# Optimization experiments

Measured on AMD Instinct MI355X. Metric: run time of the kernel, lower is better.

The kernel has to match this reference:

```python
import jax, jax.numpy as jnp
import numpy as np

B, S, H = 64, 512, 768      # batch, subtokens, BERT hidden
N, E = 128, 1024            # word-nodes per graph, directed edges per graph
GH, FH, L = 128, 256, 2     # gnn_hidden, fc_hidden, num_labels


def setup_inputs() -> dict:
    key = jax.random.key(0)
    ks = jax.random.split(key, 14)
    p = lambda k, shp: 0.02 * jax.random.normal(k, shp, jnp.float32)
    return {
        "last_hidden": jax.random.normal(ks[0], (B, S, H), jnp.float32),
        "submap": jax.random.randint(ks[1], (B, S), 0, N, dtype=jnp.int32),
        "edge_index": jax.random.randint(ks[2], (B, 2, E), 0, N, dtype=jnp.int32),
        "num_nodes": N,
        "wr": p(ks[3], (H,)), "br": jnp.zeros((), jnp.float32),
        "W1": p(ks[4], (H, GH)), "b1": jnp.zeros((GH,), jnp.float32),
        "W2": p(ks[5], (GH, GH)), "b2": jnp.zeros((GH,), jnp.float32),
        "Wf1": p(ks[6], (H + GH, FH)), "bf1": jnp.zeros((FH,), jnp.float32),
        "Wf2": p(ks[7], (FH, L)), "bf2": jnp.zeros((L,), jnp.float32),
    }


def reference(last_hidden, submap, edge_index, num_nodes,
              wr, br, W1, b1, W2, b2, Wf1, bf1, Wf2, bf2):
    Bn, Sn, Hn = last_hidden.shape
    Nn = num_nodes
    BN = Bn * Nn

    # --- per-token rationale gating ---
    gate = jax.nn.sigmoid(jnp.einsum("bsh,h->bs", last_hidden, wr) + br)  # [B,S]
    gated = last_hidden * gate[..., None]                                  # [B,S,H]

    # --- subtoken -> word-node mean pooling (batched segment mean) ---
    offs = (jnp.arange(Bn, dtype=submap.dtype) * Nn)[:, None]
    seg = (submap + offs).reshape(-1)                     # [B*S] global node ids
    flat = gated.reshape(Bn * Sn, Hn)
    sums = jax.ops.segment_sum(flat, seg, num_segments=BN)
    cnts = jax.ops.segment_sum(jnp.ones((Bn * Sn,), flat.dtype), seg, num_segments=BN)
    node_feats = sums / jnp.maximum(cnts, 1.0)[:, None]   # zeros where no subtoken maps

    # --- batched GCN message passing (self-loops + PyG gcn_norm) ---
    eoffs = (jnp.arange(Bn, dtype=edge_index.dtype) * Nn)[:, None]
    src = (edge_index[:, 0, :] + eoffs).reshape(-1)       # [B*E]
    dst = (edge_index[:, 1, :] + eoffs).reshape(-1)
    self_idx = jnp.arange(BN, dtype=src.dtype)
    src_all = jnp.concatenate([src, self_idx])
    dst_all = jnp.concatenate([dst, self_idx])
    deg = jax.ops.segment_sum(jnp.ones_like(src_all, jnp.float32), dst_all, num_segments=BN)
    dinv = jax.lax.rsqrt(deg)                             # deg >= 1 due to self-loops
    norm = dinv[src_all] * dinv[dst_all]                  # [B*E + B*N]

    def gcn_layer(x, W, b):
        h = x @ W                                         # transform first (PyG GCNConv)
        msg = h[src_all] * norm[:, None]
        out = jax.ops.segment_sum(msg, dst_all, num_segments=BN) + b
        return jax.nn.relu(out)                           # relu applied in forward()

    x = gcn_layer(node_feats, W1, b1)
    x = gcn_layer(x, W2, b2)

    # --- graph mean pool, concat with CLS, classifier head (dropout = eval identity) ---
    pooled = x.reshape(Bn, Nn, -1).mean(axis=1)           # [B,GH]
    cls_emb = last_hidden[:, 0, :]                        # [B,H]
    h = jax.nn.relu(jnp.concatenate([cls_emb, pooled], axis=1) @ Wf1 + bf1)
    return h @ Wf2 + bf2                                  # [B,num_labels]
```

## Files before the change

### kernel.cpp

```cpp
#include <hip/hip_runtime.h>
#include <math.h>

#define Bz 64
#define Sz 512
#define Hz 768
#define Nz 128
#define Ez 1024
#define GHz 128
#define FHz 256
#define Lz 2
#define BNz (Bz * Nz)

typedef short bf16x8 __attribute__((ext_vector_type(8)));
typedef float f32x4  __attribute__((ext_vector_type(4)));
typedef unsigned short ushort;

__device__ inline ushort f2b(float f) {
    union { float f; unsigned u; } v; v.f = f;
    return (ushort)((v.u + 0x7FFFu + ((v.u >> 16) & 1u)) >> 16);
}

__global__ __launch_bounds__(256) void k_stage(
        const float* __restrict__ lh, const int* __restrict__ submap,
        const float* __restrict__ wr, const float* __restrict__ br,
        const float* __restrict__ W1, const float* __restrict__ W2,
        const int* __restrict__ ei,
        ushort* __restrict__ nfb, ushort* __restrict__ W1T, ushort* __restrict__ W2T,
        int* __restrict__ rowptrG, int* __restrict__ srcsG,
        float* __restrict__ wnG, float* __restrict__ dinvG) {
    int blk = blockIdx.x, t = threadIdx.x;
    __shared__ __align__(16) char arena[12288];

    if (blk >= 8192 && blk < 8576) {
        int i = (blk - 8192) * 256 + t;
        { int k = i >> 7, n = i & 127; W1T[n * Hz + k] = f2b(W1[i]); }
        if (i < GHz * GHz) { int k = i >> 7, n = i & 127; W2T[n * GHz + k] = f2b(W2[i]); }
        return;
    }
    if (blk >= 8576) {
        int b = blk - 8576;
        int*   srcl2 = (int*)arena;
        int*   dstl2 = (int*)(arena + 4096);
        int*   hist  = (int*)(arena + 8192);
        int*   off   = (int*)(arena + 8704);
        int*   rp    = (int*)(arena + 9216);
        float* di    = (float*)(arena + 9732);
        if (t < Nz) { hist[t] = 0; off[t] = 0; }
        __syncthreads();
        #pragma unroll
        for (int j = 0; j < 4; ++j) {
            int e = t + 256 * j;
            int s = ei[b * 2 * Ez + e], d = ei[b * 2 * Ez + Ez + e];
            srcl2[e] = s; dstl2[e] = d;
            atomicAdd(&hist[d], 1);
        }
        __syncthreads();
        if (t < Nz) {
            di[t] = rsqrtf((float)hist[t] + 1.0f);
            dinvG[b * Nz + t] = di[t];
        }
        __syncthreads();
        if (t < 64) {
            int s0 = hist[2 * t], s1 = hist[2 * t + 1];
            int tot = s0 + s1, run = tot;
            #pragma unroll
            for (int o = 1; o < 64; o <<= 1) {
                int v = __shfl_up(run, o);
                if (t >= o) run += v;
            }
            int excl = run - tot;
            rp[2 * t] = excl; rp[2 * t + 1] = excl + s0;
            if (t == 63) rp[Nz] = run;
        }
        __syncthreads();
        #pragma unroll
        for (int j = 0; j < 4; ++j) {
            int e = t + 256 * j;
            int s = srcl2[e], d = dstl2[e];
            int pos = rp[d] + atomicAdd(&off[d], 1);
            srcsG[b * Ez + pos] = s;
            wnG[b * Ez + pos] = di[s] * di[d];
        }
        if (t < Nz) rowptrG[b * (Nz + 1) + t] = rp[t];
        if (t == 0) rowptrG[b * (Nz + 1) + Nz] = rp[Nz];
        return;
    }

    int b = blk >> 7, n = blk & 127;
    int lane = t & 63, wid = t >> 6;
    float* partial = (float*)arena;
    int*   list    = (int*)(arena + 9216);
    int*   lcnt    = (int*)(arena + 11264);
    if (t == 0) *lcnt = 0;
    __syncthreads();
    #pragma unroll
    for (int j = 0; j < 2; ++j) {
        int s = t + 256 * j;
        if (submap[b * Sz + s] == n) { int p = atomicAdd(lcnt, 1); list[p] = s; }
    }
    __syncthreads();
    int cnt = *lcnt;
    float brv = br[0];
    const float* wp = wr + lane * 12;
    float4 w0 = *(const float4*)&wp[0];
    float4 w1 = *(const float4*)&wp[4];
    float4 w2 = *(const float4*)&wp[8];
    float4 a0 = {0,0,0,0}, a1 = {0,0,0,0}, a2 = {0,0,0,0};
    for (int i = wid; i < cnt; i += 4) {
        const float* x = lh + (size_t)(b * Sz + list[i]) * Hz + lane * 12;
        float4 v0 = *(const float4*)&x[0];
        float4 v1 = *(const float4*)&x[4];
        float4 v2 = *(const float4*)&x[8];
        float p = v0.x*w0.x + v0.y*w0.y + v0.z*w0.z + v0.w*w0.w
                + v1.x*w1.x + v1.y*w1.y + v1.z*w1.z + v1.w*w1.w
                + v2.x*w2.x + v2.y*w2.y + v2.z*w2.z + v2.w*w2.w;
        #pragma unroll
        for (int o = 32; o > 0; o >>= 1) p += __shfl_down(p, o);
        float z = __shfl(p, 0) + brv;
        float g = 1.0f / (1.0f + __expf(-z));
        a0.x += g*v0.x; a0.y += g*v0.y; a0.z += g*v0.z; a0.w += g*v0.w;
        a1.x += g*v1.x; a1.y += g*v1.y; a1.z += g*v1.z; a1.w += g*v1.w;
        a2.x += g*v2.x; a2.y += g*v2.y; a2.z += g*v2.z; a2.w += g*v2.w;
    }
    if (wid > 0) {
        float* pp = partial + (wid - 1) * Hz + lane * 12;
        *(float4*)&pp[0] = a0; *(float4*)&pp[4] = a1; *(float4*)&pp[8] = a2;
    }
    __syncthreads();
    if (wid == 0) {
        float invc = 1.0f / fmaxf((float)cnt, 1.0f);
        #pragma unroll
        for (int m = 0; m < 3; ++m) {
            const float* pp = partial + m * Hz + lane * 12;
            float4 p0 = *(const float4*)&pp[0];
            float4 p1 = *(const float4*)&pp[4];
            float4 p2 = *(const float4*)&pp[8];
            a0.x += p0.x; a0.y += p0.y; a0.z += p0.z; a0.w += p0.w;
            a1.x += p1.x; a1.y += p1.y; a1.z += p1.z; a1.w += p1.w;
            a2.x += p2.x; a2.y += p2.y; a2.z += p2.z; a2.w += p2.w;
        }
        float o[12];
        o[0]=a0.x*invc; o[1]=a0.y*invc; o[2]=a0.z*invc;  o[3]=a0.w*invc;
        o[4]=a1.x*invc; o[5]=a1.y*invc; o[6]=a1.z*invc;  o[7]=a1.w*invc;
        o[8]=a2.x*invc; o[9]=a2.y*invc; o[10]=a2.z*invc; o[11]=a2.w*invc;
        unsigned* ob = (unsigned*)(nfb + (size_t)(b * Nz + n) * Hz + lane * 12);
        #pragma unroll
        for (int j = 0; j < 6; ++j)
            ob[j] = (unsigned)f2b(o[2*j]) | ((unsigned)f2b(o[2*j+1]) << 16);
    }
}

#define GSP 72
#define HP  132
#define XP  136
__global__ __launch_bounds__(1024) void k_gnn_fused(
        const ushort* __restrict__ nfb, const ushort* __restrict__ W1T,
        const ushort* __restrict__ W2T,
        const int* __restrict__ rowptrG, const int* __restrict__ srcsG,
        const float* __restrict__ wnG, const float* __restrict__ dinvG,
        const float* __restrict__ b1, const float* __restrict__ b2,
        const float* __restrict__ lh,
        const float* __restrict__ Wf1, const float* __restrict__ bf1,
        const float* __restrict__ Wf2, const float* __restrict__ bf2,
        float* __restrict__ outG) {
    __shared__ __align__(16) ushort As[128 * GSP];
    __shared__ __align__(16) ushort Bs[128 * GSP];
    __shared__ __align__(16) float  hL[128 * HP];
    __shared__ __align__(16) ushort xb[128 * XP];
    __shared__ int   rp[Nz + 1];
    __shared__ int   srcl[Ez];
    __shared__ float wnl[Ez];
    __shared__ float dil[Nz];
    __shared__ float wsum[16 * 128];

    int b = blockIdx.x;
    int t = threadIdx.x;
    int w = t >> 6, lane = t & 63;
    int q = lane >> 4, l16 = lane & 15;
    int wm = w >> 2, wn2 = w & 3;

    if (t < Nz + 1) rp[t] = rowptrG[b * (Nz + 1) + t];
    if (t < Nz) dil[t] = dinvG[b * Nz + t];
    srcl[t] = srcsG[b * Ez + t];
    wnl[t]  = wnG[b * Ez + t];

    int ar = t >> 3, as_ = t & 7;

    f32x4 acc[2][2];
    #pragma unroll
    for (int mf = 0; mf < 2; ++mf)
        #pragma unroll
        for (int nf = 0; nf < 2; ++nf) acc[mf][nf] = (f32x4){0, 0, 0, 0};

    const ushort* Ab = nfb + (size_t)b * Nz * Hz;
    uint4 apre, bpre;
    auto loadT1 = [&](int k0) {
        apre = *(const uint4*)&Ab[(size_t)ar * Hz + k0 + as_ * 8];
        bpre = *(const uint4*)&W1T[(size_t)ar * Hz + k0 + as_ * 8];
    };
    loadT1(0);
    for (int k0 = 0; k0 < Hz; k0 += 64) {
        __syncthreads();
        *(uint4*)&As[ar * GSP + as_ * 8] = apre;
        *(uint4*)&Bs[ar * GSP + as_ * 8] = bpre;
        if (k0 + 64 < Hz) loadT1(k0 + 64);
        __syncthreads();
        #pragma unroll
        for (int ks = 0; ks < 64; ks += 32)
            #pragma unroll
            for (int mf = 0; mf < 2; ++mf) {
                bf16x8 af = *(const bf16x8*)&As[(wm * 32 + mf * 16 + l16) * GSP + ks + q * 8];
                #pragma unroll
                for (int nf = 0; nf < 2; ++nf) {
                    bf16x8 bv = *(const bf16x8*)&Bs[(wn2 * 32 + nf * 16 + l16) * GSP + ks + q * 8];
                    acc[mf][nf] = __builtin_amdgcn_mfma_f32_16x16x32_bf16(af, bv, acc[mf][nf], 0, 0, 0);
                }
            }
    }
    #pragma unroll
    for (int mf = 0; mf < 2; ++mf)
        #pragma unroll
        for (int nf = 0; nf < 2; ++nf)
            #pragma unroll
            for (int r = 0; r < 4; ++r)
                hL[(wm * 32 + mf * 16 + q * 4 + r) * HP + wn2 * 32 + nf * 16 + l16] = acc[mf][nf][r];
    __syncthreads();

    float* inL  = (float*)As;
    float* redA = inL + 896;
    if (t < 224) ((float4*)inL)[t] = ((const float4*)(lh + (size_t)b * Sz * Hz))[t];
    __syncthreads();

    if (w < 8) {
        float b1v0 = b1[lane], b1v1 = b1[lane + 64];
        for (int d = w; d < Nz; d += 8) {
            float dd = dil[d];
            float a0 = hL[d * HP + lane] * dd * dd;
            float a1 = hL[d * HP + lane + 64] * dd * dd;
            float c0 = 0.f, c1 = 0.f;
            int i = rp[d], pe = rp[d + 1];
            for (; i + 4 <= pe; i += 4) {
                int s0_ = srcl[i], s1_ = srcl[i+1], s2_ = srcl[i+2], s3_ = srcl[i+3];
                float n0 = wnl[i], n1 = wnl[i+1], n2 = wnl[i+2], n3 = wnl[i+3];
                float h0a = hL[s0_*HP+lane], h0b = hL[s0_*HP+lane+64];
                float h1a = hL[s1_*HP+lane], h1b = hL[s1_*HP+lane+64];
                float h2a = hL[s2_*HP+lane], h2b = hL[s2_*HP+lane+64];
                float h3a = hL[s3_*HP+lane], h3b = hL[s3_*HP+lane+64];
                a0 += h0a*n0; a1 += h0b*n0; c0 += h1a*n1; c1 += h1b*n1;
                a0 += h2a*n2; a1 += h2b*n2; c0 += h3a*n3; c1 += h3b*n3;
            }
            for (; i < pe; ++i) {
                int s_ = srcl[i]; float nm = wnl[i];
                a0 += hL[s_*HP+lane]*nm; a1 += hL[s_*HP+lane+64]*nm;
            }
            a0 += c0; a1 += c1;
            xb[d * XP + lane]      = f2b(fmaxf(a0 + b1v0, 0.0f));
            xb[d * XP + lane + 64] = f2b(fmaxf(a1 + b1v1, 0.0f));
        }
    } else {
        int tt = t - 512;
        int f2 = tt & 127, kq = tt >> 7;
        const float* Wp = Wf1 + (size_t)(kq * 192) * FHz + f2 * 2;
        const float* ip = inL + kq * 192;
        float ax = 0.f, ay = 0.f;
        #pragma unroll 8
        for (int k = 0; k < 192; ++k) {
            float iv = ip[k];
            float2 wv = *(const float2*)&Wp[(size_t)k * FHz];
            ax += iv * wv.x; ay += iv * wv.y;
        }
        redA[kq * 256 + f2 * 2]     = ax;
        redA[kq * 256 + f2 * 2 + 1] = ay;
    }
    __syncthreads();

    #pragma unroll
    for (int mf = 0; mf < 2; ++mf)
        #pragma unroll
        for (int nf = 0; nf < 2; ++nf) acc[mf][nf] = (f32x4){0, 0, 0, 0};
    for (int k0 = 0; k0 < GHz; k0 += 64) {
        __syncthreads();
        *(uint4*)&Bs[ar * GSP + as_ * 8] = *(const uint4*)&W2T[(size_t)ar * GHz + k0 + as_ * 8];
        __syncthreads();
        #pragma unroll
        for (int ks = 0; ks < 64; ks += 32)
            #pragma unroll
            for (int mf = 0; mf < 2; ++mf) {
                bf16x8 af = *(const bf16x8*)&xb[(wm * 32 + mf * 16 + l16) * XP + k0 + ks + q * 8];
                #pragma unroll
                for (int nf = 0; nf < 2; ++nf) {
                    bf16x8 bv = *(const bf16x8*)&Bs[(wn2 * 32 + nf * 16 + l16) * GSP + ks + q * 8];
                    acc[mf][nf] = __builtin_amdgcn_mfma_f32_16x16x32_bf16(af, bv, acc[mf][nf], 0, 0, 0);
                }
            }
    }
    __syncthreads();
    #pragma unroll
    for (int mf = 0; mf < 2; ++mf)
        #pragma unroll
        for (int nf = 0; nf < 2; ++nf)
            #pragma unroll
            for (int r = 0; r < 4; ++r)
                hL[(wm * 32 + mf * 16 + q * 4 + r) * HP + wn2 * 32 + nf * 16 + l16] = acc[mf][nf][r];
    __syncthreads();

    float b2v0 = b2[lane], b2v1 = b2[lane + 64];
    float p0 = 0.0f, p1 = 0.0f;
    for (int d = w; d < Nz; d += 16) {
        float dd = dil[d];
        float a0 = hL[d * HP + lane] * dd * dd;
        float a1 = hL[d * HP + lane + 64] * dd * dd;
        float c0 = 0.f, c1 = 0.f;
        int i = rp[d], pe = rp[d + 1];
        for (; i + 4 <= pe; i += 4) {
            int s0_ = srcl[i], s1_ = srcl[i+1], s2_ = srcl[i+2], s3_ = srcl[i+3];
            float n0 = wnl[i], n1 = wnl[i+1], n2 = wnl[i+2], n3 = wnl[i+3];
            float h0a = hL[s0_*HP+lane], h0b = hL[s0_*HP+lane+64];
            float h1a = hL[s1_*HP+lane], h1b = hL[s1_*HP+lane+64];
            float h2a = hL[s2_*HP+lane], h2b = hL[s2_*HP+lane+64];
            float h3a = hL[s3_*HP+lane], h3b = hL[s3_*HP+lane+64];
            a0 += h0a*n0; a1 += h0b*n0; c0 += h1a*n1; c1 += h1b*n1;
            a0 += h2a*n2; a1 += h2b*n2; c0 += h3a*n3; c1 += h3b*n3;
        }
        for (; i < pe; ++i) {
            int s_ = srcl[i]; float nm = wnl[i];
            a0 += hL[s_*HP+lane]*nm; a1 += hL[s_*HP+lane+64]*nm;
        }
        a0 += c0; a1 += c1;
        p0 += fmaxf(a0 + b2v0, 0.0f);
        p1 += fmaxf(a1 + b2v1, 0.0f);
    }
    wsum[w * 128 + lane]      = p0;
    wsum[w * 128 + lane + 64] = p1;
    __syncthreads();
    if (t < Nz) {
        float s = 0.0f;
        #pragma unroll
        for (int ww = 0; ww < 16; ++ww) s += wsum[ww * 128 + t];
        inL[Hz + t] = s * (1.0f / Nz);
    }
    __syncthreads();

    float* redB  = (float*)Bs;
    float* hvecL = ((float*)Bs) + 2048;
    {
        int f2 = t & 127, kc8 = t >> 7;
        const float* Wp = Wf1 + (size_t)(Hz + kc8 * 16) * FHz + f2 * 2;
        const float* ip = inL + Hz + kc8 * 16;
        float ax = 0.f, ay = 0.f;
        #pragma unroll
        for (int k = 0; k < 16; ++k) {
            float iv = ip[k];
            float2 wv = *(const float2*)&Wp[(size_t)k * FHz];
            ax += iv * wv.x; ay += iv * wv.y;
        }
        redB[kc8 * 256 + f2 * 2]     = ax;
        redB[kc8 * 256 + f2 * 2 + 1] = ay;
    }
    __syncthreads();
    if (t < 128) {
        float sx = bf1[2 * t], sy = bf1[2 * t + 1];
        #pragma unroll
        for (int m = 0; m < 4; ++m) { sx += redA[m * 256 + 2 * t]; sy += redA[m * 256 + 2 * t + 1]; }
        #pragma unroll
        for (int m = 0; m < 8; ++m) { sx += redB[m * 256 + 2 * t]; sy += redB[m * 256 + 2 * t + 1]; }
        hvecL[2 * t]     = fmaxf(sx, 0.0f);
        hvecL[2 * t + 1] = fmaxf(sy, 0.0f);
    }
    __syncthreads();
    if (t < 128) {
        int l = t >> 6, j0 = t & 63;
        float s = 0.0f;
        #pragma unroll
        for (int m = 0; m < 4; ++m) s += hvecL[j0 + 64 * m] * Wf2[(j0 + 64 * m) * Lz + l];
        #pragma unroll
        for (int o = 32; o > 0; o >>= 1) s += __shfl_down(s, o);
        if (j0 == 0) outG[b * Lz + l] = s + bf2[l];
    }
}

extern "C" void kernel_launch(void* const* d_in, const int* in_sizes, int n_in,
                              void* d_out, int out_size, void* d_ws, size_t ws_size,
                              hipStream_t stream) {
    const float* lh     = (const float*)d_in[0];
    const int*   submap = (const int*)d_in[1];
    const int*   ei     = (const int*)d_in[2];
    const float* wr  = (const float*)d_in[4];
    const float* br  = (const float*)d_in[5];
    const float* W1  = (const float*)d_in[6];
    const float* b1  = (const float*)d_in[7];
    const float* W2  = (const float*)d_in[8];
    const float* b2  = (const float*)d_in[9];
    const float* Wf1 = (const float*)d_in[10];
    const float* bf1 = (const float*)d_in[11];
    const float* Wf2 = (const float*)d_in[12];
    const float* bf2 = (const float*)d_in[13];
    float* out = (float*)d_out;

    char* p = (char*)d_ws;
    ushort* nfb  = (ushort*)p;  p += (size_t)BNz * Hz * 2;
    ushort* W1T  = (ushort*)p;  p += (size_t)Hz * GHz * 2;
    ushort* W2T  = (ushort*)p;  p += (size_t)GHz * GHz * 2;
    int*    rowptrG = (int*)p;  p += (size_t)Bz * (Nz + 1) * 4;
    int*    srcsG   = (int*)p;  p += (size_t)Bz * Ez * 4;
    float*  wnG     = (float*)p; p += (size_t)Bz * Ez * 4;
    float*  dinvG   = (float*)p; p += (size_t)Bz * Nz * 4;

    k_stage<<<8192 + 384 + 64, 256, 0, stream>>>(lh, submap, wr, br, W1, W2, ei,
                                                 nfb, W1T, W2T, rowptrG, srcsG, wnG, dinvG);
    k_gnn_fused<<<Bz, 1024, 0, stream>>>(nfb, W1T, W2T, rowptrG, srcsG, wnG, dinvG,
                                         b1, b2, lh, Wf1, bf1, Wf2, bf2, out);
}
```

Baseline: 207.5 us.

## Move CLS classifier matmul to staging kernel and restructure fused GNN kernel

```diff
diff --git a/kernel.cpp b/kernel.cpp
--- a/kernel.cpp
+++ b/kernel.cpp
@@ -24,21 +24,75 @@
         const float* __restrict__ lh, const int* __restrict__ submap,
         const float* __restrict__ wr, const float* __restrict__ br,
         const float* __restrict__ W1, const float* __restrict__ W2,
-        const int* __restrict__ ei,
+        const int* __restrict__ ei, const float* __restrict__ Wf1,
         ushort* __restrict__ nfb, ushort* __restrict__ W1T, ushort* __restrict__ W2T,
         int* __restrict__ rowptrG, int* __restrict__ srcsG,
-        float* __restrict__ wnG, float* __restrict__ dinvG) {
+        float* __restrict__ wnG, float* __restrict__ dinvG,
+        float* __restrict__ redA_G) {
     int blk = blockIdx.x, t = threadIdx.x;
-    __shared__ __align__(16) char arena[12288];
-
-    if (blk >= 8192 && blk < 8576) {
-        int i = (blk - 8192) * 256 + t;
-        { int k = i >> 7, n = i & 127; W1T[n * Hz + k] = f2b(W1[i]); }
-        if (i < GHz * GHz) { int k = i >> 7, n = i & 127; W2T[n * GHz + k] = f2b(W2[i]); }
+    __shared__ __align__(16) char arena[17408];
+
+    if (blk < 64) {
+        int b = blk;
+        float* clsL = (float*)arena;
+        float* pA   = (float*)(arena + 3072);
+        clsL[t]       = lh[(size_t)b * Sz * Hz + t];
+        clsL[t + 256] = lh[(size_t)b * Sz * Hz + t + 256];
+        clsL[t + 512] = lh[(size_t)b * Sz * Hz + t + 512];
+        __syncthreads();
+        int f2 = t & 127, kc = t >> 7;
+        const float* Wp = Wf1 + (size_t)(kc * 384) * FHz + f2 * 2;
+        const float* ip = clsL + kc * 384;
+        float ax = 0.f, ay = 0.f;
+        #pragma unroll 8
+        for (int k = 0; k < 384; ++k) {
+            float iv = ip[k];
+            float2 wv = *(const float2*)&Wp[(size_t)k * FHz];
+            ax += iv * wv.x; ay += iv * wv.y;
+        }
+        pA[kc * 256 + f2 * 2]     = ax;
+        pA[kc * 256 + f2 * 2 + 1] = ay;
+        __syncthreads();
+        if (t < 128) {
+            float2 o;
+            o.x = pA[2 * t]     + pA[256 + 2 * t];
+            o.y = pA[2 * t + 1] + pA[256 + 2 * t + 1];
+            *(float2*)&redA_G[b * 256 + 2 * t] = o;
+        }
         return;
     }
-    if (blk >= 8576) {
-        int b = blk - 8576;
+    if (blk < 78) {
+        ushort* sT = (ushort*)arena;
+        bool isW2 = (blk >= 76);
+        int T = isW2 ? (blk - 76) : (blk - 64);
+        int k0 = T * 64;
+        const float* Wsrc = isW2 ? W2 : W1;
+        #pragma unroll
+        for (int j = 0; j < 32; ++j) {
+            int idx = j * 256 + t;
+            int k = idx >> 7, n = idx & 127;
+            sT[k * 136 + n] = f2b(Wsrc[(size_t)(k0 + k) * 128 + n]);
+        }
+        __syncthreads();
+        if (isW2) {
+            #pragma unroll
+            for (int j = 0; j < 32; ++j) {
+                int idx = j * 256 + t;
+                int n = idx >> 6, k = idx & 63;
+                W2T[n * GHz + k0 + k] = sT[k * 136 + n];
+            }
+        } else {
+            #pragma unroll
+            for (int j = 0; j < 32; ++j) {
+                int idx = j * 256 + t;
+                int n = idx >> 6, k = idx & 63;
+                W1T[n * Hz + k0 + k] = sT[k * 136 + n];
+            }
+        }
+        return;
+    }
+    if (blk < 142) {
+        int b = blk - 78;
         int*   srcl2 = (int*)arena;
         int*   dstl2 = (int*)(arena + 4096);
         int*   hist  = (int*)(arena + 8192);
@@ -86,7 +140,8 @@
         return;
     }
 
-    int b = blk >> 7, n = blk & 127;
+    int g = blk - 142;
+    int b = g >> 7, n = g & 127;
     int lane = t & 63, wid = t >> 6;
     float* partial = (float*)arena;
     int*   list    = (int*)(arena + 9216);
@@ -117,10 +172,10 @@
         #pragma unroll
         for (int o = 32; o > 0; o >>= 1) p += __shfl_down(p, o);
         float z = __shfl(p, 0) + brv;
-        float g = 1.0f / (1.0f + __expf(-z));
-        a0.x += g*v0.x; a0.y += g*v0.y; a0.z += g*v0.z; a0.w += g*v0.w;
-        a1.x += g*v1.x; a1.y += g*v1.y; a1.z += g*v1.z; a1.w += g*v1.w;
-        a2.x += g*v2.x; a2.y += g*v2.y; a2.z += g*v2.z; a2.w += g*v2.w;
+        float g2 = 1.0f / (1.0f + __expf(-z));
+        a0.x += g2*v0.x; a0.y += g2*v0.y; a0.z += g2*v0.z; a0.w += g2*v0.w;
+        a1.x += g2*v1.x; a1.y += g2*v1.y; a1.z += g2*v1.z; a1.w += g2*v1.w;
+        a2.x += g2*v2.x; a2.y += g2*v2.y; a2.z += g2*v2.z; a2.w += g2*v2.w;
     }
     if (wid > 0) {
         float* pp = partial + (wid - 1) * Hz + lane * 12;
@@ -151,184 +206,198 @@
 }
 
 #define GSP 72
-#define HP  132
-#define XP  136
+#define O_BS    18432
+#define O_HL    36864
+#define O_XB    102400
+#define O_RP    137216
+#define O_SRC   137744
+#define O_WN    141840
+#define O_DIL   145936
+#define O_POOL  146448
+#define O_HVEC  146960
 __global__ __launch_bounds__(1024) void k_gnn_fused(
         const ushort* __restrict__ nfb, const ushort* __restrict__ W1T,
         const ushort* __restrict__ W2T,
         const int* __restrict__ rowptrG, const int* __restrict__ srcsG,
         const float* __restrict__ wnG, const float* __restrict__ dinvG,
         const float* __restrict__ b1, const float* __restrict__ b2,
-        const float* __restrict__ lh,
+        const float* __restrict__ redA_G,
         const float* __restrict__ Wf1, const float* __restrict__ bf1,
         const float* __restrict__ Wf2, const float* __restrict__ bf2,
         float* __restrict__ outG) {
-    __shared__ __align__(16) ushort As[128 * GSP];
-    __shared__ __align__(16) ushort Bs[128 * GSP];
-    __shared__ __align__(16) float  hL[128 * HP];
-    __shared__ __align__(16) ushort xb[128 * XP];
-    __shared__ int   rp[Nz + 1];
-    __shared__ int   srcl[Ez];
-    __shared__ float wnl[Ez];
-    __shared__ float dil[Nz];
-    __shared__ float wsum[16 * 128];
+    __shared__ __align__(16) char Lar[147984];
+    ushort* As   = (ushort*)(Lar);
+    ushort* Bs   = (ushort*)(Lar + O_BS);
+    ushort* W2s  = (ushort*)(Lar);
+    float*  hLf  = (float*)(Lar + O_HL);
+    ushort* xb   = (ushort*)(Lar + O_XB);
+    float*  wsum = (float*)(Lar + O_XB);
+    float*  redB = (float*)(Lar + O_XB + 8192);
+    int*    rp   = (int*)(Lar + O_RP);
+    int*    srcl = (int*)(Lar + O_SRC);
+    float*  wnl  = (float*)(Lar + O_WN);
+    float*  dil  = (float*)(Lar + O_DIL);
+    float*  pooledL = (float*)(Lar + O_POOL);
+    float*  hvecL   = (float*)(Lar + O_HVEC);
+    const float2* hL2 = (const float2*)hLf;
 
     int b = blockIdx.x;
     int t = threadIdx.x;
     int w = t >> 6, lane = t & 63;
     int q = lane >> 4, l16 = lane & 15;
     int wm = w >> 2, wn2 = w & 3;
+    int kq = q * 8;
+    int ar = t >> 3, as_ = t & 7;
+
+    const ushort* Ab = nfb + (size_t)b * Nz * Hz;
+    uint4 aA, bA, aB, bB;
+    aA = *(const uint4*)&Ab[(size_t)ar * Hz + 0  + as_ * 8];
+    bA = *(const uint4*)&W1T[(size_t)ar * Hz + 0  + as_ * 8];
+    aB = *(const uint4*)&Ab[(size_t)ar * Hz + 64 + as_ * 8];
+    bB = *(const uint4*)&W1T[(size_t)ar * Hz + 64 + as_ * 8];
+    __builtin_amdgcn_sched_barrier(0);
 
     if (t < Nz + 1) rp[t] = rowptrG[b * (Nz + 1) + t];
     if (t < Nz) dil[t] = dinvG[b * Nz + t];
     srcl[t] = srcsG[b * Ez + t];
     wnl[t]  = wnG[b * Ez + t];
 
-    int ar = t >> 3, as_ = t & 7;
-
-    f32x4 acc[2][2];
-    #pragma unroll
-    for (int mf = 0; mf < 2; ++mf)
-        #pragma unroll
-        for (int nf = 0; nf < 2; ++nf) acc[mf][nf] = (f32x4){0, 0, 0, 0};
-
-    const ushort* Ab = nfb + (size_t)b * Nz * Hz;
-    uint4 apre, bpre;
-    auto loadT1 = [&](int k0) {
-        apre = *(const uint4*)&Ab[(size_t)ar * Hz + k0 + as_ * 8];
-        bpre = *(const uint4*)&W1T[(size_t)ar * Hz + k0 + as_ * 8];
+    f32x4 acc00 = {0,0,0,0}, acc01 = {0,0,0,0}, acc10 = {0,0,0,0}, acc11 = {0,0,0,0};
+    auto mfma_tile = [&]() {
+        #pragma unroll
+        for (int ks = 0; ks < 64; ks += 32) {
+            bf16x8 af0 = *(const bf16x8*)&As[(wm * 32 +      l16) * GSP + ks + kq];
+            bf16x8 af1 = *(const bf16x8*)&As[(wm * 32 + 16 + l16) * GSP + ks + kq];
+            bf16x8 bv0 = *(const bf16x8*)&Bs[(wn2 * 32 +      l16) * GSP + ks + kq];
+            bf16x8 bv1 = *(const bf16x8*)&Bs[(wn2 * 32 + 16 + l16) * GSP + ks + kq];
+            acc00 = __builtin_amdgcn_mfma_f32_16x16x32_bf16(af0, bv0, acc00, 0, 0, 0);
+            acc01 = __builtin_amdgcn_mfma_f32_16x16x32_bf16(af0, bv1, acc01, 0, 0, 0);
+            acc10 = __builtin_amdgcn_mfma_f32_16x16x32_bf16(af1, bv0, acc10, 0, 0, 0);
+            acc11 = __builtin_amdgcn_mfma_f32_16x16x32_bf16(af1, bv1, acc11, 0, 0, 0);
+        }
     };
-    loadT1(0);
-    for (int k0 = 0; k0 < Hz; k0 += 64) {
-        __syncthreads();
-        *(uint4*)&As[ar * GSP + as_ * 8] = apre;
-        *(uint4*)&Bs[ar * GSP + as_ * 8] = bpre;
-        if (k0 + 64 < Hz) loadT1(k0 + 64);
-        __syncthreads();
-        #pragma unroll
-        for (int ks = 0; ks < 64; ks += 32)
-            #pragma unroll
-            for (int mf = 0; mf < 2; ++mf) {
-                bf16x8 af = *(const bf16x8*)&As[(wm * 32 + mf * 16 + l16) * GSP + ks + q * 8];
-                #pragma unroll
-                for (int nf = 0; nf < 2; ++nf) {
-                    bf16x8 bv = *(const bf16x8*)&Bs[(wn2 * 32 + nf * 16 + l16) * GSP + ks + q * 8];
-                    acc[mf][nf] = __builtin_amdgcn_mfma_f32_16x16x32_bf16(af, bv, acc[mf][nf], 0, 0, 0);
-                }
-            }
-    }
-    #pragma unroll
-    for (int mf = 0; mf < 2; ++mf)
-        #pragma unroll
-        for (int nf = 0; nf < 2; ++nf)
-            #pragma unroll
-            for (int r = 0; r < 4; ++r)
-                hL[(wm * 32 + mf * 16 + q * 4 + r) * HP + wn2 * 32 + nf * 16 + l16] = acc[mf][nf][r];
-    __syncthreads();
-
-    float* inL  = (float*)As;
-    float* redA = inL + 896;
-    if (t < 224) ((float4*)inL)[t] = ((const float4*)(lh + (size_t)b * Sz * Hz))[t];
-    __syncthreads();
-
-    if (w < 8) {
-        float b1v0 = b1[lane], b1v1 = b1[lane + 64];
-        for (int d = w; d < Nz; d += 8) {
-            float dd = dil[d];
-            float a0 = hL[d * HP + lane] * dd * dd;
-            float a1 = hL[d * HP + lane + 64] * dd * dd;
-            float c0 = 0.f, c1 = 0.f;
-            int i = rp[d], pe = rp[d + 1];
-            for (; i + 4 <= pe; i += 4) {
-                int s0_ = srcl[i], s1_ = srcl[i+1], s2_ = srcl[i+2], s3_ = srcl[i+3];
-                float n0 = wnl[i], n1 = wnl[i+1], n2 = wnl[i+2], n3 = wnl[i+3];
-                float h0a = hL[s0_*HP+lane], h0b = hL[s0_*HP+lane+64];
-                float h1a = hL[s1_*HP+lane], h1b = hL[s1_*HP+lane+64];
-                float h2a = hL[s2_*HP+lane], h2b = hL[s2_*HP+lane+64];
-                float h3a = hL[s3_*HP+lane], h3b = hL[s3_*HP+lane+64];
-                a0 += h0a*n0; a1 += h0b*n0; c0 += h1a*n1; c1 += h1b*n1;
-                a0 += h2a*n2; a1 += h2b*n2; c0 += h3a*n3; c1 += h3b*n3;
-            }
-            for (; i < pe; ++i) {
-                int s_ = srcl[i]; float nm = wnl[i];
-                a0 += hL[s_*HP+lane]*nm; a1 += hL[s_*HP+lane+64]*nm;
-            }
-            a0 += c0; a1 += c1;
-            xb[d * XP + lane]      = f2b(fmaxf(a0 + b1v0, 0.0f));
-            xb[d * XP + lane + 64] = f2b(fmaxf(a1 + b1v1, 0.0f));
-        }
-    } else {
-        int tt = t - 512;
-        int f2 = tt & 127, kq = tt >> 7;
-        const float* Wp = Wf1 + (size_t)(kq * 192) * FHz + f2 * 2;
-        const float* ip = inL + kq * 192;
-        float ax = 0.f, ay = 0.f;
-        #pragma unroll 8
-        for (int k = 0; k < 192; ++k) {
-            float iv = ip[k];
-            float2 wv = *(const float2*)&Wp[(size_t)k * FHz];
-            ax += iv * wv.x; ay += iv * wv.y;
-        }
-        redA[kq * 256 + f2 * 2]     = ax;
-        redA[kq * 256 + f2 * 2 + 1] = ay;
-    }
-    __syncthreads();
-
-    #pragma unroll
-    for (int mf = 0; mf < 2; ++mf)
-        #pragma unroll
-        for (int nf = 0; nf < 2; ++nf) acc[mf][nf] = (f32x4){0, 0, 0, 0};
-    for (int k0 = 0; k0 < GHz; k0 += 64) {
-        __syncthreads();
-        *(uint4*)&Bs[ar * GSP + as_ * 8] = *(const uint4*)&W2T[(size_t)ar * GHz + k0 + as_ * 8];
-        __syncthreads();
-        #pragma unroll
-        for (int ks = 0; ks < 64; ks += 32)
-            #pragma unroll
-            for (int mf = 0; mf < 2; ++mf) {
-                bf16x8 af = *(const bf16x8*)&xb[(wm * 32 + mf * 16 + l16) * XP + k0 + ks + q * 8];
-                #pragma unroll
-                for (int nf = 0; nf < 2; ++nf) {
-                    bf16x8 bv = *(const bf16x8*)&Bs[(wn2 * 32 + nf * 16 + l16) * GSP + ks + q * 8];
-                    acc[mf][nf] = __builtin_amdgcn_mfma_f32_16x16x32_bf16(af, bv, acc[mf][nf], 0, 0, 0);
-                }
-            }
-    }
-    __syncthreads();
-    #pragma unroll
-    for (int mf = 0; mf < 2; ++mf)
-        #pragma unroll
-        for (int nf = 0; nf < 2; ++nf)
-            #pragma unroll
-            for (int r = 0; r < 4; ++r)
-                hL[(wm * 32 + mf * 16 + q * 4 + r) * HP + wn2 * 32 + nf * 16 + l16] = acc[mf][nf][r];
-    __syncthreads();
-
-    float b2v0 = b2[lane], b2v1 = b2[lane + 64];
-    float p0 = 0.0f, p1 = 0.0f;
+
+    for (int k0 = 0; k0 < Hz; k0 += 128) {
+        __syncthreads();
+        *(uint4*)&As[ar * GSP + as_ * 8] = aA;
+        *(uint4*)&Bs[ar * GSP + as_ * 8] = bA;
+        if (k0 + 128 < Hz) {
+            aA = *(const uint4*)&Ab[(size_t)ar * Hz + k0 + 128 + as_ * 8];
+            bA = *(const uint4*)&W1T[(size_t)ar * Hz + k0 + 128 + as_ * 8];
+        }
+        __builtin_amdgcn_sched_barrier(0);
+        __syncthreads();
+        mfma_tile();
+        __syncthreads();
+        *(uint4*)&As[ar * GSP + as_ * 8] = aB;
+        *(uint4*)&Bs[ar * GSP + as_ * 8] = bB;
+        if (k0 + 192 < Hz) {
+            aB = *(const uint4*)&Ab[(size_t)ar * Hz + k0 + 192 + as_ * 8];
+            bB = *(const uint4*)&W1T[(size_t)ar * Hz + k0 + 192 + as_ * 8];
+        }
+        __builtin_amdgcn_sched_barrier(0);
+        __syncthreads();
+        mfma_tile();
+    }
+    {
+        int c0 = wn2 * 32 + l16, c1 = c0 + 16;
+        #pragma unroll
+        for (int r = 0; r < 4; ++r) {
+            int r0 = (wm * 32 + q * 4 + r) * 128, r1 = r0 + 16 * 128;
+            hLf[r0 + (c0 & 63) * 2 + (c0 >> 6)] = acc00[r];
+            hLf[r0 + (c1 & 63) * 2 + (c1 >> 6)] = acc01[r];
+            hLf[r1 + (c0 & 63) * 2 + (c0 >> 6)] = acc10[r];
+            hLf[r1 + (c1 & 63) * 2 + (c1 >> 6)] = acc11[r];
+        }
+    }
+    __syncthreads();
+
+    int n0 = t >> 4, sg = t & 15;
+    uint4 w2r0 = *(const uint4*)&W2T[n0 * GHz + sg * 8];
+    uint4 w2r1 = *(const uint4*)&W2T[(n0 + 64) * GHz + sg * 8];
+    __builtin_amdgcn_sched_barrier(0);
+
+    float bx0 = b1[lane], bx1 = b1[lane + 64];
     for (int d = w; d < Nz; d += 16) {
         float dd = dil[d];
-        float a0 = hL[d * HP + lane] * dd * dd;
-        float a1 = hL[d * HP + lane + 64] * dd * dd;
+        float2 hv = hL2[d * 64 + lane];
+        float a0 = hv.x * dd * dd, a1 = hv.y * dd * dd;
         float c0 = 0.f, c1 = 0.f;
         int i = rp[d], pe = rp[d + 1];
         for (; i + 4 <= pe; i += 4) {
             int s0_ = srcl[i], s1_ = srcl[i+1], s2_ = srcl[i+2], s3_ = srcl[i+3];
-            float n0 = wnl[i], n1 = wnl[i+1], n2 = wnl[i+2], n3 = wnl[i+3];
-            float h0a = hL[s0_*HP+lane], h0b = hL[s0_*HP+lane+64];
-            float h1a = hL[s1_*HP+lane], h1b = hL[s1_*HP+lane+64];
-            float h2a = hL[s2_*HP+lane], h2b = hL[s2_*HP+lane+64];
-            float h3a = hL[s3_*HP+lane], h3b = hL[s3_*HP+lane+64];
-            a0 += h0a*n0; a1 += h0b*n0; c0 += h1a*n1; c1 += h1b*n1;
-            a0 += h2a*n2; a1 += h2b*n2; c0 += h3a*n3; c1 += h3b*n3;
+            float m0 = wnl[i], m1 = wnl[i+1], m2 = wnl[i+2], m3 = wnl[i+3];
+            float2 h0 = hL2[s0_ * 64 + lane], h1 = hL2[s1_ * 64 + lane];
+            float2 h2 = hL2[s2_ * 64 + lane], h3 = hL2[s3_ * 64 + lane];
+            a0 += h0.x*m0; a1 += h0.y*m0; c0 += h1.x*m1; c1 += h1.y*m1;
+            a0 += h2.x*m2; a1 += h2.y*m2; c0 += h3.x*m3; c1 += h3.y*m3;
         }
         for (; i < pe; ++i) {
             int s_ = srcl[i]; float nm = wnl[i];
-            a0 += hL[s_*HP+lane]*nm; a1 += hL[s_*HP+lane+64]*nm;
+            float2 h = hL2[s_ * 64 + lane];
+            a0 += h.x * nm; a1 += h.y * nm;
         }
         a0 += c0; a1 += c1;
-        p0 += fmaxf(a0 + b2v0, 0.0f);
-        p1 += fmaxf(a1 + b2v1, 0.0f);
+        xb[d * 136 + lane]      = f2b(fmaxf(a0 + bx0, 0.0f));
+        xb[d * 136 + lane + 64] = f2b(fmaxf(a1 + bx1, 0.0f));
+    }
+    __syncthreads();
+
+    *(uint4*)((char*)W2s + n0 * 272 + sg * 16)        = w2r0;
+    *(uint4*)((char*)W2s + (n0 + 64) * 272 + sg * 16) = w2r1;
+    __syncthreads();
+
+    acc00 = (f32x4){0,0,0,0}; acc01 = (f32x4){0,0,0,0};
+    acc10 = (f32x4){0,0,0,0}; acc11 = (f32x4){0,0,0,0};
+    #pragma unroll
+    for (int ks = 0; ks < GHz; ks += 32) {
+        bf16x8 af0 = *(const bf16x8*)&xb[(wm * 32 +      l16) * 136 + ks + kq];
+        bf16x8 af1 = *(const bf16x8*)&xb[(wm * 32 + 16 + l16) * 136 + ks + kq];
+        bf16x8 bv0 = *(const bf16x8*)&W2s[(wn2 * 32 +      l16) * 136 + ks + kq];
+        bf16x8 bv1 = *(const bf16x8*)&W2s[(wn2 * 32 + 16 + l16) * 136 + ks + kq];
+        acc00 = __builtin_amdgcn_mfma_f32_16x16x32_bf16(af0, bv0, acc00, 0, 0, 0);
+        acc01 = __builtin_amdgcn_mfma_f32_16x16x32_bf16(af0, bv1, acc01, 0, 0, 0);
+        acc10 = __builtin_amdgcn_mfma_f32_16x16x32_bf16(af1, bv0, acc10, 0, 0, 0);
+        acc11 = __builtin_amdgcn_mfma_f32_16x16x32_bf16(af1, bv1, acc11, 0, 0, 0);
+    }
+    __syncthreads();
+    {
+        int c0 = wn2 * 32 + l16, c1 = c0 + 16;
+        #pragma unroll
+        for (int r = 0; r < 4; ++r) {
+            int r0 = (wm * 32 + q * 4 + r) * 128, r1 = r0 + 16 * 128;
+            hLf[r0 + (c0 & 63) * 2 + (c0 >> 6)] = acc00[r];
+            hLf[r0 + (c1 & 63) * 2 + (c1 >> 6)] = acc01[r];
+            hLf[r1 + (c0 & 63) * 2 + (c0 >> 6)] = acc10[r];
+            hLf[r1 + (c1 & 63) * 2 + (c1 >> 6)] = acc11[r];
+        }
+    }
+    __syncthreads();
+
+    float by0 = b2[lane], by1 = b2[lane + 64];
+    float p0 = 0.0f, p1 = 0.0f;
+    for (int d = w; d < Nz; d += 16) {
+        float dd = dil[d];
+        float2 hv = hL2[d * 64 + lane];
+        float a0 = hv.x * dd * dd, a1 = hv.y * dd * dd;
+        float c0 = 0.f, c1 = 0.f;
+        int i = rp[d], pe = rp[d + 1];
+        for (; i + 4 <= pe; i += 4) {
+            int s0_ = srcl[i], s1_ = srcl[i+1], s2_ = srcl[i+2], s3_ = srcl[i+3];
+            float m0 = wnl[i], m1 = wnl[i+1], m2 = wnl[i+2], m3 = wnl[i+3];
+            float2 h0 = hL2[s0_ * 64 + lane], h1 = hL2[s1_ * 64 + lane];
+            float2 h2 = hL2[s2_ * 64 + lane], h3 = hL2[s3_ * 64 + lane];
+            a0 += h0.x*m0; a1 += h0.y*m0; c0 += h1.x*m1; c1 += h1.y*m1;
+            a0 += h2.x*m2; a1 += h2.y*m2; c0 += h3.x*m3; c1 += h3.y*m3;
+        }
+        for (; i < pe; ++i) {
+            int s_ = srcl[i]; float nm = wnl[i];
+            float2 h = hL2[s_ * 64 + lane];
+            a0 += h.x * nm; a1 += h.y * nm;
+        }
+        a0 += c0; a1 += c1;
+        p0 += fmaxf(a0 + by0, 0.0f);
+        p1 += fmaxf(a1 + by1, 0.0f);
     }
     wsum[w * 128 + lane]      = p0;
     wsum[w * 128 + lane + 64] = p1;
@@ -337,16 +406,14 @@
         float s = 0.0f;
         #pragma unroll
         for (int ww = 0; ww < 16; ++ww) s += wsum[ww * 128 + t];
-        inL[Hz + t] = s * (1.0f / Nz);
-    }
-    __syncthreads();
-
-    float* redB  = (float*)Bs;
-    float* hvecL = ((float*)Bs) + 2048;
+        pooledL[t] = s * (1.0f / Nz);
+    }
+    __syncthreads();
+
     {
         int f2 = t & 127, kc8 = t >> 7;
         const float* Wp = Wf1 + (size_t)(Hz + kc8 * 16) * FHz + f2 * 2;
-        const float* ip = inL + Hz + kc8 * 16;
+        const float* ip = pooledL + kc8 * 16;
         float ax = 0.f, ay = 0.f;
         #pragma unroll
         for (int k = 0; k < 16; ++k) {
@@ -359,9 +426,8 @@
     }
     __syncthreads();
     if (t < 128) {
-        float sx = bf1[2 * t], sy = bf1[2 * t + 1];
-        #pragma unroll
-        for (int m = 0; m < 4; ++m) { sx += redA[m * 256 + 2 * t]; sy += redA[m * 256 + 2 * t + 1]; }
+        float sx = bf1[2 * t]     + redA_G[b * 256 + 2 * t];
+        float sy = bf1[2 * t + 1] + redA_G[b * 256 + 2 * t + 1];
         #pragma unroll
         for (int m = 0; m < 8; ++m) { sx += redB[m * 256 + 2 * t]; sy += redB[m * 256 + 2 * t + 1]; }
         hvecL[2 * t]     = fmaxf(sx, 0.0f);
@@ -405,9 +471,10 @@
     int*    srcsG   = (int*)p;  p += (size_t)Bz * Ez * 4;
     float*  wnG     = (float*)p; p += (size_t)Bz * Ez * 4;
     float*  dinvG   = (float*)p; p += (size_t)Bz * Nz * 4;
-
-    k_stage<<<8192 + 384 + 64, 256, 0, stream>>>(lh, submap, wr, br, W1, W2, ei,
-                                                 nfb, W1T, W2T, rowptrG, srcsG, wnG, dinvG);
+    float*  redA_G  = (float*)p; p += (size_t)Bz * FHz * 4;
+
+    k_stage<<<142 + 8192, 256, 0, stream>>>(lh, submap, wr, br, W1, W2, ei, Wf1,
+                                            nfb, W1T, W2T, rowptrG, srcsG, wnG, dinvG, redA_G);
     k_gnn_fused<<<Bz, 1024, 0, stream>>>(nfb, W1T, W2T, rowptrG, srcsG, wnG, dinvG,
-                                         b1, b2, lh, Wf1, bf1, Wf2, bf2, out);
+                                         b1, b2, redA_G, Wf1, bf1, Wf2, bf2, out);
 }
```

Measured after the change: 203.5 us, median of 2. About the same (-1.9%).
